# Optimization experiments

Hardware: AMD Instinct MI355X
Metric: run time of the kernel (lower is better)

The kernel has to match this reference:

```python
import jax, jax.numpy as jnp
import numpy as np

B, N, D, D_OUT = 4, 512, 48, 48

def setup_inputs() -> dict:
    key = jax.random.key(0)
    ks = jax.random.split(key, 7)
    s1 = 1.0 / np.sqrt(2 * D)
    s2 = 1.0 / np.sqrt(2 * D)
    s3 = 1.0 / np.sqrt(D)
    return {
        "x": jax.random.normal(ks[0], (B, N, D), dtype=jnp.float32),
        "W1": jax.random.uniform(ks[1], (2 * D, 2 * D), jnp.float32, -s1, s1),
        "b1": jax.random.uniform(ks[2], (2 * D,), jnp.float32, -s1, s1),
        "W2": jax.random.uniform(ks[3], (2 * D, D), jnp.float32, -s2, s2),
        "b2": jax.random.uniform(ks[4], (D,), jnp.float32, -s2, s2),
        "W3": jax.random.uniform(ks[5], (D, D_OUT), jnp.float32, -s3, s3),
        "b3": jax.random.uniform(ks[6], (D_OUT,), jnp.float32, -s3, s3),
    }

def reference(x, W1, b1, W2, b2, W3, b3):
    # x: [B, N, D]
    Bn, Nn, Dn = x.shape
    xi = jnp.broadcast_to(x[:, :, None, :], (Bn, Nn, Nn, Dn))  # row i
    xj = jnp.broadcast_to(x[:, None, :, :], (Bn, Nn, Nn, Dn))  # col j
    pair = jnp.concatenate([xi, xj], axis=-1)  # [B,N,N,2D]
    h = jax.nn.gelu(pair @ W1 + b1, approximate=False)
    h = jax.nn.gelu(h @ W2 + b2, approximate=False)
    pair_out = h @ W3 + b3  # [B,N,N,d_out]
    mask = jnp.triu(jnp.ones((Nn, Nn), dtype=bool), 1)  # j > i masked
    pair_out = jnp.where(mask[None, :, :, None], 0.0, pair_out)
    w = jnp.linalg.norm(pair_out, axis=-1)  # [B,N,N]
    w = jnp.where(mask[None, :, :], -1e9, w)
    w = jax.nn.softmax(w, axis=-1)
    return jnp.einsum('bnj,bnjd->bnd', w, pair_out)
```

## Files before the change

### kernel.cpp

```cpp
#include <hip/hip_runtime.h>
#include <hip/hip_bf16.h>


constexpr int BATCH = 4;
constexpr int SEQ   = 512;
constexpr int DIM   = 48;
constexpr int DIM2  = 96;
constexpr int CH    = 64;

constexpr int AW  = 104;
constexpr int HW  = 72;

typedef short short4v __attribute__((ext_vector_type(4)));
typedef short short8v __attribute__((ext_vector_type(8)));
typedef float float4v __attribute__((ext_vector_type(4)));

#define MFMA16(a, b, c) __builtin_amdgcn_mfma_f32_16x16x32_bf16(a, b, c, 0, 0, 0)

__device__ __forceinline__ float gelu_fast(float x) {
    float z  = fabsf(x) * 0.70710678118654752f;
    float t  = __builtin_amdgcn_rcpf(fmaf(0.3275911f, z, 1.0f));
    float p  =             1.061405429f;
    p = fmaf(p, t, -1.453152027f);
    p = fmaf(p, t,  1.421413741f);
    p = fmaf(p, t, -0.284496736f);
    p = fmaf(p, t,  0.254829592f);
    p = p * t;
    float e  = __builtin_amdgcn_exp2f(z * z * -1.4426950408889634f);
    float er = fmaf(-p, e, 1.0f);
    er = copysignf(er, x);
    float hx = 0.5f * x;
    return fmaf(hx, er, hx);
}
__device__ __forceinline__ short f2bf(float v) {
    unsigned u = __float_as_uint(v);
    u += 0x7FFFu + ((u >> 16) & 1u);
    return (short)(u >> 16);
}
constexpr float LOG2E = 1.4426950408889634f;

__global__ __launch_bounds__(192) void uv_kernel(
    const float* __restrict__ x, const float* __restrict__ W1,
    const float* __restrict__ b1, float* __restrict__ U, float* __restrict__ V)
{
    __shared__ float sxT[DIM * 4];
    const int t = threadIdx.x;
    const int row0 = blockIdx.x * 4;
    if (t < DIM * 4) {
        int r = t / DIM, m = t - r * DIM;
        sxT[m * 4 + r] = x[(row0 + r) * DIM + m];
    }
    __syncthreads();
    const bool isU = (t < DIM2);
    const int  k   = isU ? t : (t - DIM2);
    const float* Wcol = W1 + (isU ? 0 : DIM * DIM2) + k;
    float binit = isU ? b1[k] : 0.0f;
    float a0 = binit, a1 = binit, a2 = binit, a3 = binit;
    #pragma unroll 8
    for (int m = 0; m < DIM; ++m) {
        float wv = Wcol[m * DIM2];
        const float4 xa = *(const float4*)&sxT[m * 4];
        a0 = fmaf(wv, xa.x, a0); a1 = fmaf(wv, xa.y, a1);
        a2 = fmaf(wv, xa.z, a2); a3 = fmaf(wv, xa.w, a3);
    }
    float* dst = isU ? U : V;
    dst[(row0 + 0) * DIM2 + k] = a0; dst[(row0 + 1) * DIM2 + k] = a1;
    dst[(row0 + 2) * DIM2 + k] = a2; dst[(row0 + 3) * DIM2 + k] = a3;
}

__global__ __launch_bounds__(256, 4) void pair_kernel(
    const float* __restrict__ U, const float* __restrict__ V,
    const float* __restrict__ W2, const float* __restrict__ b2,
    const float* __restrict__ W3, const float* __restrict__ b3,
    float* __restrict__ out)
{
    __shared__ __align__(16) short sA[CH * AW];
    __shared__ __align__(16) short sW2T[DIM * AW];
    __shared__ __align__(16) short sH[CH * HW];
    __shared__ __align__(16) short sW3T[DIM * HW];
    __shared__ __align__(16) float sUi[DIM2];
    __shared__ __align__(16) float sB2f[DIM];
    __shared__ __align__(16) float sB3f[DIM];
    __shared__ __align__(16) float sNrm[CH];

    const int t   = threadIdx.x;
    const int bid = blockIdx.x;
    const int b   = bid & (BATCH - 1);
    const int i   = (SEQ - 1) - (bid >> 2);
    const int rowbase = b * SEQ + i;

    for (int idx = t; idx < DIM2 * DIM; idx += 256) {
        int k = idx / DIM, n = idx - k * DIM;
        sW2T[n * AW + k] = f2bf(W2[idx]);
    }
    for (int idx = t; idx < DIM * DIM; idx += 256) {
        int k = idx / DIM, n = idx - k * DIM;
        sW3T[n * HW + k] = f2bf(W3[idx]);
    }
    for (int idx = t; idx < DIM * 16; idx += 256)
        sW3T[(idx >> 4) * HW + 48 + (idx & 15)] = 0;
    for (int idx = t; idx < CH * 16; idx += 256)
        sH[(idx >> 4) * HW + 48 + (idx & 15)] = 0;
    if (t < DIM2) sUi[t] = U[rowbase * DIM2 + t];
    if (t < DIM)  { sB2f[t] = b2[t]; sB3f[t] = b3[t]; }
    __syncthreads();

    const int lane = t & 63;
    const int w    = t >> 6;
    const int col  = lane & 15;
    const int quad = lane >> 4;
    const int qo   = quad * 8;
    const int m4   = w * 16 + col;
    const int rbase = w * 16 + quad * 4;

    const int pr = t >> 2;
    const int pq = t & 3;
    float4 uu[6];
    #pragma unroll
    for (int k = 0; k < 6; ++k) uu[k] = *(const float4*)&sUi[(pq + 4 * k) * 4];

    float acc0 = 0.f, acc1 = 0.f, acc2 = 0.f;
    float m_run = -1e30f, l_run = 0.0f;

    for (int j0 = 0; j0 <= i; j0 += CH) {
        const int JJ = min(CH, i + 1 - j0);

        {
            const float* Vb = V + (b * SEQ + j0 + pr) * DIM2 + pq * 4;
            #pragma unroll
            for (int k = 0; k < 6; ++k) {
                const float4 vv = *(const float4*)(Vb + 16 * k);
                short4v o;
                o[0] = f2bf(gelu_fast(uu[k].x + vv.x));
                o[1] = f2bf(gelu_fast(uu[k].y + vv.y));
                o[2] = f2bf(gelu_fast(uu[k].z + vv.z));
                o[3] = f2bf(gelu_fast(uu[k].w + vv.w));
                *(short4v*)&sA[pr * AW + (pq + 4 * k) * 4] = o;
            }
        }
        __syncthreads();

        {
            const short* arow = &sA[m4 * AW + qo];
            short8v a0 = *(const short8v*)(arow + 0);
            short8v a1 = *(const short8v*)(arow + 32);
            short8v a2 = *(const short8v*)(arow + 64);
            float4v c0 = {0.f,0.f,0.f,0.f}, c1 = c0, c2 = c0;
            const short* w2b = &sW2T[col * AW + qo];
            c0 = MFMA16(a0, *(const short8v*)(w2b + 0),          c0);
            c0 = MFMA16(a1, *(const short8v*)(w2b + 32),         c0);
            c0 = MFMA16(a2, *(const short8v*)(w2b + 64),         c0);
            c1 = MFMA16(a0, *(const short8v*)(w2b + 16*AW + 0),  c1);
            c1 = MFMA16(a1, *(const short8v*)(w2b + 16*AW + 32), c1);
            c1 = MFMA16(a2, *(const short8v*)(w2b + 16*AW + 64), c1);
            c2 = MFMA16(a0, *(const short8v*)(w2b + 32*AW + 0),  c2);
            c2 = MFMA16(a1, *(const short8v*)(w2b + 32*AW + 32), c2);
            c2 = MFMA16(a2, *(const short8v*)(w2b + 32*AW + 64), c2);
            float bb0 = sB2f[col], bb1 = sB2f[16 + col], bb2 = sB2f[32 + col];
            #pragma unroll
            for (int r = 0; r < 4; ++r) {
                sH[(rbase + r) * HW +  0 + col] = f2bf(gelu_fast(c0[r] + bb0));
                sH[(rbase + r) * HW + 16 + col] = f2bf(gelu_fast(c1[r] + bb1));
                sH[(rbase + r) * HW + 32 + col] = f2bf(gelu_fast(c2[r] + bb2));
            }
        }
        __syncthreads();

        float4v p0, p1, p2;
        {
            const short* hrw = &sH[m4 * HW + qo];
            short8v a0 = *(const short8v*)(hrw + 0);
            short8v a1 = *(const short8v*)(hrw + 32);
            float4v c0 = {0.f,0.f,0.f,0.f}, c1 = c0, c2 = c0;
            const short* w3b = &sW3T[col * HW + qo];
            c0 = MFMA16(a0, *(const short8v*)(w3b + 0),          c0);
            c0 = MFMA16(a1, *(const short8v*)(w3b + 32),         c0);
            c1 = MFMA16(a0, *(const short8v*)(w3b + 16*HW + 0),  c1);
            c1 = MFMA16(a1, *(const short8v*)(w3b + 16*HW + 32), c1);
            c2 = MFMA16(a0, *(const short8v*)(w3b + 32*HW + 0),  c2);
            c2 = MFMA16(a1, *(const short8v*)(w3b + 32*HW + 32), c2);
            float bb0 = sB3f[col], bb1 = sB3f[16 + col], bb2 = sB3f[32 + col];
            #pragma unroll
            for (int r = 0; r < 4; ++r) {
                p0[r] = c0[r] + bb0; p1[r] = c1[r] + bb1; p2[r] = c2[r] + bb2;
                float ss = p0[r]*p0[r] + p1[r]*p1[r] + p2[r]*p2[r];
                ss += __shfl_xor(ss, 1);
                ss += __shfl_xor(ss, 2);
                ss += __shfl_xor(ss, 4);
                ss += __shfl_xor(ss, 8);
                if (col == 0) sNrm[rbase + r] = sqrtf(ss);
            }
        }
        __syncthreads();

        {
            float nr = (lane < JJ) ? sNrm[lane] : -1e30f;
            float mx = nr;
            mx = fmaxf(mx, __shfl_xor(mx, 1));  mx = fmaxf(mx, __shfl_xor(mx, 2));
            mx = fmaxf(mx, __shfl_xor(mx, 4));  mx = fmaxf(mx, __shfl_xor(mx, 8));
            mx = fmaxf(mx, __shfl_xor(mx, 16)); mx = fmaxf(mx, __shfl_xor(mx, 32));
            float newm = fmaxf(m_run, mx);
            float e = (lane < JJ) ? __builtin_amdgcn_exp2f((nr - newm) * LOG2E) : 0.0f;
            float s = e;
            s += __shfl_xor(s, 1);  s += __shfl_xor(s, 2);
            s += __shfl_xor(s, 4);  s += __shfl_xor(s, 8);
            s += __shfl_xor(s, 16); s += __shfl_xor(s, 32);
            float sc = __builtin_amdgcn_exp2f((m_run - newm) * LOG2E);
            l_run = fmaf(l_run, sc, s);
            m_run = newm;
            acc0 *= sc; acc1 *= sc; acc2 *= sc;
            #pragma unroll
            for (int r = 0; r < 4; ++r) {
                float er = __shfl(e, rbase + r);
                acc0 = fmaf(er, p0[r], acc0);
                acc1 = fmaf(er, p1[r], acc1);
                acc2 = fmaf(er, p2[r], acc2);
            }
        }
    }

    acc0 += __shfl_xor(acc0, 16); acc0 += __shfl_xor(acc0, 32);
    acc1 += __shfl_xor(acc1, 16); acc1 += __shfl_xor(acc1, 32);
    acc2 += __shfl_xor(acc2, 16); acc2 += __shfl_xor(acc2, 32);
    float* sRed = (float*)sA;
    __syncthreads();
    if (lane < 16) {
        sRed[w * DIM + lane]      = acc0;
        sRed[w * DIM + 16 + lane] = acc1;
        sRed[w * DIM + 32 + lane] = acc2;
    }
    __syncthreads();
    if (t < DIM) {
        float o = (sRed[t] + sRed[DIM + t] + sRed[2*DIM + t] + sRed[3*DIM + t]) / l_run;
        out[rowbase * DIM + t] = o;
    }
}

extern "C" void kernel_launch(void* const* d_in, const int* in_sizes, int n_in,
                              void* d_out, int out_size, void* d_ws, size_t ws_size,
                              hipStream_t stream) {
    const float* x  = (const float*)d_in[0];
    const float* W1 = (const float*)d_in[1];
    const float* b1 = (const float*)d_in[2];
    const float* W2 = (const float*)d_in[3];
    const float* b2 = (const float*)d_in[4];
    const float* W3 = (const float*)d_in[5];
    const float* b3 = (const float*)d_in[6];
    float* out = (float*)d_out;

    float* U = (float*)d_ws;
    float* V = U + BATCH * SEQ * DIM2;

    uv_kernel<<<BATCH * SEQ / 4, 192, 0, stream>>>(x, W1, b1, U, V);
    pair_kernel<<<BATCH * SEQ, 256, 0, stream>>>(U, V, W2, b2, W3, b3, out);
}
```

Measured before the change: 128.7 us.

## Use tanh GELU, keep weight fragments in registers, shrink shared memory

Result: faster. 114.9 us (-10.7%).

```diff
diff --git a/kernel.cpp b/kernel.cpp
--- a/kernel.cpp
+++ b/kernel.cpp
@@ -11,31 +11,26 @@
 constexpr int AW  = 104;
 constexpr int HW  = 72;
 
-typedef short short4v __attribute__((ext_vector_type(4)));
 typedef short short8v __attribute__((ext_vector_type(8)));
 typedef float float4v __attribute__((ext_vector_type(4)));
+typedef unsigned int uint2v __attribute__((ext_vector_type(2)));
 
 #define MFMA16(a, b, c) __builtin_amdgcn_mfma_f32_16x16x32_bf16(a, b, c, 0, 0, 0)
 
-__device__ __forceinline__ float gelu_fast(float x) {
-    float z  = fabsf(x) * 0.70710678118654752f;
-    float t  = __builtin_amdgcn_rcpf(fmaf(0.3275911f, z, 1.0f));
-    float p  =             1.061405429f;
-    p = fmaf(p, t, -1.453152027f);
-    p = fmaf(p, t,  1.421413741f);
-    p = fmaf(p, t, -0.284496736f);
-    p = fmaf(p, t,  0.254829592f);
-    p = p * t;
-    float e  = __builtin_amdgcn_exp2f(z * z * -1.4426950408889634f);
-    float er = fmaf(-p, e, 1.0f);
-    er = copysignf(er, x);
-    float hx = 0.5f * x;
-    return fmaf(hx, er, hx);
-}
-__device__ __forceinline__ short f2bf(float v) {
-    unsigned u = __float_as_uint(v);
-    u += 0x7FFFu + ((u >> 16) & 1u);
-    return (short)(u >> 16);
+__device__ __forceinline__ float gelu_tanh(float x) {
+    float u = x * x;
+    float q = fmaf(0.10294537f, u, 2.3022077f);
+    float e = __builtin_amdgcn_exp2f(x * q);
+    float r = __builtin_amdgcn_rcpf(e + 1.0f);
+    return fmaf(-x, r, x);
+}
+__device__ __forceinline__ short f2bf1(float v) {
+    return (short)((__float_as_uint(v) + 0x8000u) >> 16);
+}
+__device__ __forceinline__ unsigned pack_bf16x2(float a, float b) {
+    unsigned ua = __float_as_uint(a) + 0x8000u;
+    unsigned ub = __float_as_uint(b) + 0x8000u;
+    return __builtin_amdgcn_perm(ub, ua, 0x07060302u);
 }
 constexpr float LOG2E = 1.4426950408889634f;
 
@@ -74,36 +69,17 @@
     const float* __restrict__ W3, const float* __restrict__ b3,
     float* __restrict__ out)
 {
-    __shared__ __align__(16) short sA[CH * AW];
-    __shared__ __align__(16) short sW2T[DIM * AW];
-    __shared__ __align__(16) short sH[CH * HW];
-    __shared__ __align__(16) short sW3T[DIM * HW];
-    __shared__ __align__(16) float sUi[DIM2];
-    __shared__ __align__(16) float sB2f[DIM];
-    __shared__ __align__(16) float sB3f[DIM];
-    __shared__ __align__(16) float sNrm[CH];
+    __shared__ __align__(16) char smem[23168];
+    short* sA   = (short*)smem;
+    short* sH   = (short*)(smem + 13312);
+    float* sUi  = (float*)(smem + 22528);
+    float* sNrm = (float*)(smem + 22912);
 
     const int t   = threadIdx.x;
     const int bid = blockIdx.x;
     const int b   = bid & (BATCH - 1);
     const int i   = (SEQ - 1) - (bid >> 2);
     const int rowbase = b * SEQ + i;
-
-    for (int idx = t; idx < DIM2 * DIM; idx += 256) {
-        int k = idx / DIM, n = idx - k * DIM;
-        sW2T[n * AW + k] = f2bf(W2[idx]);
-    }
-    for (int idx = t; idx < DIM * DIM; idx += 256) {
-        int k = idx / DIM, n = idx - k * DIM;
-        sW3T[n * HW + k] = f2bf(W3[idx]);
-    }
-    for (int idx = t; idx < DIM * 16; idx += 256)
-        sW3T[(idx >> 4) * HW + 48 + (idx & 15)] = 0;
-    for (int idx = t; idx < CH * 16; idx += 256)
-        sH[(idx >> 4) * HW + 48 + (idx & 15)] = 0;
-    if (t < DIM2) sUi[t] = U[rowbase * DIM2 + t];
-    if (t < DIM)  { sB2f[t] = b2[t]; sB3f[t] = b3[t]; }
-    __syncthreads();
 
     const int lane = t & 63;
     const int w    = t >> 6;
@@ -113,11 +89,42 @@
     const int m4   = w * 16 + col;
     const int rbase = w * 16 + quad * 4;
 
+    for (int idx = t; idx < DIM2 * DIM; idx += 256) {
+        int k = idx / DIM, n = idx - k * DIM;
+        sA[n * AW + k] = f2bf1(W2[idx]);
+    }
+    for (int idx = t; idx < DIM * DIM; idx += 256) {
+        int k = idx / DIM, n = idx - k * DIM;
+        sH[n * HW + k] = f2bf1(W3[idx]);
+    }
+    for (int idx = t; idx < CH * 16; idx += 256)
+        sH[(idx >> 4) * HW + 48 + (idx & 15)] = 0;
+    if (t < DIM2) sUi[t] = U[rowbase * DIM2 + t];
+    __syncthreads();
+
+    const short* w2b = sA + col * AW + qo;
+    const short8v w200 = *(const short8v*)(w2b + 0);
+    const short8v w201 = *(const short8v*)(w2b + 32);
+    const short8v w202 = *(const short8v*)(w2b + 64);
+    const short8v w210 = *(const short8v*)(w2b + 16*AW + 0);
+    const short8v w211 = *(const short8v*)(w2b + 16*AW + 32);
+    const short8v w212 = *(const short8v*)(w2b + 16*AW + 64);
+    const short8v w220 = *(const short8v*)(w2b + 32*AW + 0);
+    const short8v w221 = *(const short8v*)(w2b + 32*AW + 32);
+    const short8v w222 = *(const short8v*)(w2b + 32*AW + 64);
+    const short* w3b = sH + col * HW + qo;
+    const short8v w300 = *(const short8v*)(w3b + 0);
+    const short8v w301 = *(const short8v*)(w3b + 32);
+    const short8v w310 = *(const short8v*)(w3b + 16*HW + 0);
+    const short8v w311 = *(const short8v*)(w3b + 16*HW + 32);
+    const short8v w320 = *(const short8v*)(w3b + 32*HW + 0);
+    const short8v w321 = *(const short8v*)(w3b + 32*HW + 32);
+    const float bb20 = b2[col], bb21 = b2[16 + col], bb22 = b2[32 + col];
+    const float bb30 = b3[col], bb31 = b3[16 + col], bb32 = b3[32 + col];
+    __syncthreads();
+
     const int pr = t >> 2;
     const int pq = t & 3;
-    float4 uu[6];
-    #pragma unroll
-    for (int k = 0; k < 6; ++k) uu[k] = *(const float4*)&sUi[(pq + 4 * k) * 4];
 
     float acc0 = 0.f, acc1 = 0.f, acc2 = 0.f;
     float m_run = -1e30f, l_run = 0.0f;
@@ -128,14 +135,17 @@
         {
             const float* Vb = V + (b * SEQ + j0 + pr) * DIM2 + pq * 4;
             #pragma unroll
-            for (int k = 0; k < 6; ++k) {
-                const float4 vv = *(const float4*)(Vb + 16 * k);
-                short4v o;
-                o[0] = f2bf(gelu_fast(uu[k].x + vv.x));
-                o[1] = f2bf(gelu_fast(uu[k].y + vv.y));
-                o[2] = f2bf(gelu_fast(uu[k].z + vv.z));
-                o[3] = f2bf(gelu_fast(uu[k].w + vv.w));
-                *(short4v*)&sA[pr * AW + (pq + 4 * k) * 4] = o;
+            for (int kk = 0; kk < 6; ++kk) {
+                const float4 vv = *(const float4*)(Vb + 16 * kk);
+                const float4 uu = *(const float4*)&sUi[(pq + 4 * kk) * 4];
+                float g0 = gelu_tanh(uu.x + vv.x);
+                float g1 = gelu_tanh(uu.y + vv.y);
+                float g2 = gelu_tanh(uu.z + vv.z);
+                float g3 = gelu_tanh(uu.w + vv.w);
+                uint2v o;
+                o.x = pack_bf16x2(g0, g1);
+                o.y = pack_bf16x2(g2, g3);
+                *(uint2v*)&sA[pr * AW + (pq + 4 * kk) * 4] = o;
             }
         }
         __syncthreads();
@@ -146,22 +156,14 @@
             short8v a1 = *(const short8v*)(arow + 32);
             short8v a2 = *(const short8v*)(arow + 64);
             float4v c0 = {0.f,0.f,0.f,0.f}, c1 = c0, c2 = c0;
-            const short* w2b = &sW2T[col * AW + qo];
-            c0 = MFMA16(a0, *(const short8v*)(w2b + 0),          c0);
-            c0 = MFMA16(a1, *(const short8v*)(w2b + 32),         c0);
-            c0 = MFMA16(a2, *(const short8v*)(w2b + 64),         c0);
-            c1 = MFMA16(a0, *(const short8v*)(w2b + 16*AW + 0),  c1);
-            c1 = MFMA16(a1, *(const short8v*)(w2b + 16*AW + 32), c1);
-            c1 = MFMA16(a2, *(const short8v*)(w2b + 16*AW + 64), c1);
-            c2 = MFMA16(a0, *(const short8v*)(w2b + 32*AW + 0),  c2);
-            c2 = MFMA16(a1, *(const short8v*)(w2b + 32*AW + 32), c2);
-            c2 = MFMA16(a2, *(const short8v*)(w2b + 32*AW + 64), c2);
-            float bb0 = sB2f[col], bb1 = sB2f[16 + col], bb2 = sB2f[32 + col];
+            c0 = MFMA16(a0, w200, c0); c0 = MFMA16(a1, w201, c0); c0 = MFMA16(a2, w202, c0);
+            c1 = MFMA16(a0, w210, c1); c1 = MFMA16(a1, w211, c1); c1 = MFMA16(a2, w212, c1);
+            c2 = MFMA16(a0, w220, c2); c2 = MFMA16(a1, w221, c2); c2 = MFMA16(a2, w222, c2);
             #pragma unroll
             for (int r = 0; r < 4; ++r) {
-                sH[(rbase + r) * HW +  0 + col] = f2bf(gelu_fast(c0[r] + bb0));
-                sH[(rbase + r) * HW + 16 + col] = f2bf(gelu_fast(c1[r] + bb1));
-                sH[(rbase + r) * HW + 32 + col] = f2bf(gelu_fast(c2[r] + bb2));
+                sH[(rbase + r) * HW +  0 + col] = f2bf1(gelu_tanh(c0[r] + bb20));
+                sH[(rbase + r) * HW + 16 + col] = f2bf1(gelu_tanh(c1[r] + bb21));
+                sH[(rbase + r) * HW + 32 + col] = f2bf1(gelu_tanh(c2[r] + bb22));
             }
         }
         __syncthreads();
@@ -172,17 +174,12 @@
             short8v a0 = *(const short8v*)(hrw + 0);
             short8v a1 = *(const short8v*)(hrw + 32);
             float4v c0 = {0.f,0.f,0.f,0.f}, c1 = c0, c2 = c0;
-            const short* w3b = &sW3T[col * HW + qo];
-            c0 = MFMA16(a0, *(const short8v*)(w3b + 0),          c0);
-            c0 = MFMA16(a1, *(const short8v*)(w3b + 32),         c0);
-            c1 = MFMA16(a0, *(const short8v*)(w3b + 16*HW + 0),  c1);
-            c1 = MFMA16(a1, *(const short8v*)(w3b + 16*HW + 32), c1);
-            c2 = MFMA16(a0, *(const short8v*)(w3b + 32*HW + 0),  c2);
-            c2 = MFMA16(a1, *(const short8v*)(w3b + 32*HW + 32), c2);
-            float bb0 = sB3f[col], bb1 = sB3f[16 + col], bb2 = sB3f[32 + col];
+            c0 = MFMA16(a0, w300, c0); c0 = MFMA16(a1, w301, c0);
+            c1 = MFMA16(a0, w310, c1); c1 = MFMA16(a1, w311, c1);
+            c2 = MFMA16(a0, w320, c2); c2 = MFMA16(a1, w321, c2);
             #pragma unroll
             for (int r = 0; r < 4; ++r) {
-                p0[r] = c0[r] + bb0; p1[r] = c1[r] + bb1; p2[r] = c2[r] + bb2;
+                p0[r] = c0[r] + bb30; p1[r] = c1[r] + bb31; p2[r] = c2[r] + bb32;
                 float ss = p0[r]*p0[r] + p1[r]*p1[r] + p2[r]*p2[r];
                 ss += __shfl_xor(ss, 1);
                 ss += __shfl_xor(ss, 2);
```
